# Performance work log

Hardware: AMD Instinct MI355X
Metric: run time of the kernel (lower is better)

The kernel has to match this reference:

```python
import jax, jax.numpy as jnp
import numpy as np
import itertools

BINS_NUM = 35
BINS_SIZE = 9
ORDERS = (2, 3, 4, 5)

def _comb_idx(n, k):
    # combinations with replacement of indices 0..n-1, shape [ncomb, k]
    return np.array(list(itertools.combinations_with_replacement(range(n), k)), dtype=np.int32)

_COMB = {k: _comb_idx(BINS_SIZE, k) for k in ORDERS}


def setup_inputs() -> dict:
    key = jax.random.key(0)
    x = jax.random.normal(key, (1024, BINS_NUM * BINS_SIZE), dtype=jnp.float32)
    return {"x": x}


def reference(x) -> jnp.ndarray:
    B = x.shape[0]
    bins = x.reshape(B, BINS_NUM, BINS_SIZE)          # [B, 35, 9]
    parts = [bins]                                     # 'origin' slice first
    for k in ORDERS:
        idx = jnp.asarray(_COMB[k])                    # [ncomb_k, k]
        gathered = bins[:, :, idx]                     # [B, 35, ncomb_k, k]
        parts.append(jnp.prod(gathered, axis=-1))      # [B, 35, ncomb_k]
    # per-bin concat [origin, de2, de3, de4, de5], then flatten bins -> matches
    # torch's outer concat over bins since bin is the leading concat axis here.
    out = jnp.concatenate(parts, axis=-1)              # [B, 35, 2001]
    return out.reshape(B, -1)                          # [B, 70035]
```

## Files before the change

### kernel.cpp

```cpp
#include <hip/hip_runtime.h>

#define NBIN 35
#define BSZ 9
#define NOUT_PER_BIN 2001

struct PackTab { unsigned pk[NOUT_PER_BIN]; };

constexpr PackTab make_tab() {
    PackTab t{};
    int p = 0;
    constexpr unsigned S = 9;
    for (unsigned a = 0; a < 9; ++a)
        t.pk[p++] = a | (S << 4) | (S << 8) | (S << 12) | (S << 16);
    for (unsigned a = 0; a < 9; ++a)
        for (unsigned b = a; b < 9; ++b)
            t.pk[p++] = a | (b << 4) | (S << 8) | (S << 12) | (S << 16);
    for (unsigned a = 0; a < 9; ++a)
        for (unsigned b = a; b < 9; ++b)
            for (unsigned c = b; c < 9; ++c)
                t.pk[p++] = a | (b << 4) | (c << 8) | (S << 12) | (S << 16);
    for (unsigned a = 0; a < 9; ++a)
        for (unsigned b = a; b < 9; ++b)
            for (unsigned c = b; c < 9; ++c)
                for (unsigned d = c; d < 9; ++d)
                    t.pk[p++] = a | (b << 4) | (c << 8) | (d << 12) | (S << 16);
    for (unsigned a = 0; a < 9; ++a)
        for (unsigned b = a; b < 9; ++b)
            for (unsigned c = b; c < 9; ++c)
                for (unsigned d = c; d < 9; ++d)
                    for (unsigned e = d; e < 9; ++e)
                        t.pk[p++] = a | (b << 4) | (c << 8) | (d << 12) | (e << 16);
    return t;
}

__constant__ PackTab g_tab = make_tab();

__global__ __launch_bounds__(256) void poly_expand_kernel(
        const float* __restrict__ x, float* __restrict__ out, int ntask) {
    __shared__ float vs[4][12];
    const int wave = threadIdx.x >> 6;
    const int lane = threadIdx.x & 63;
    const int task = blockIdx.x * 4 + wave;
    const bool valid = task < ntask;

    if (valid && lane < 10) {
        vs[wave][lane] = (lane < 9) ? x[(size_t)task * BSZ + lane] : 1.0f;
    }
    __syncthreads();
    if (!valid) return;

    const float* v = vs[wave];
    const size_t base = (size_t)task * NOUT_PER_BIN;

    for (int j0 = 0; j0 < NOUT_PER_BIN; j0 += 64) {
        const int j = j0 + lane;
        if (j < NOUT_PER_BIN) {
            const unsigned pk = g_tab.pk[j];
            float p = v[pk & 15u];
            p *= v[(pk >> 4) & 15u];
            p *= v[(pk >> 8) & 15u];
            p *= v[(pk >> 12) & 15u];
            p *= v[(pk >> 16) & 15u];
            out[base + j] = p;
        }
    }
}

extern "C" void kernel_launch(void* const* d_in, const int* in_sizes, int n_in,
                              void* d_out, int out_size, void* d_ws, size_t ws_size,
                              hipStream_t stream) {
    const float* x = (const float*)d_in[0];
    float* out = (float*)d_out;
    const int B = in_sizes[0] / (NBIN * BSZ);
    const int ntask = B * NBIN;
    const int blocks = (ntask + 3) / 4;
    poly_expand_kernel<<<blocks, 256, 0, stream>>>(x, out, ntask);
}
```

Baseline: 60.61 us.

## Compute monomials per-lane with compile-time indices and transpose through LDS

Each lane now owns one bin-task and keeps its 9 values in registers. It evaluates every monomial with indices fixed at compile time, so the constant-table lookups and dynamic LDS indexing go away. Results are staged in a padded LDS tile, transposed, and written out as 16-byte vector stores. The 2001 outputs are split into 9 slices handled by separate waves. This trades heavy code unrolling, instruction-cache pressure and extra LDS traffic for fewer table reads and wider global stores, on a kernel that is write-bandwidth bound.

```diff
diff --git a/kernel.cpp b/kernel.cpp
--- a/kernel.cpp
+++ b/kernel.cpp
@@ -1,78 +1,143 @@
 #include <hip/hip_runtime.h>
+#include <utility>
 
-#define NBIN 35
-#define BSZ 9
-#define NOUT_PER_BIN 2001
+#define NPB  2001
+#define ROWW 65
 
-struct PackTab { unsigned pk[NOUT_PER_BIN]; };
+#define WAVE_SYNC() asm volatile("s_waitcnt lgkmcnt(0)" ::: "memory")
 
-constexpr PackTab make_tab() {
-    PackTab t{};
-    int p = 0;
-    constexpr unsigned S = 9;
-    for (unsigned a = 0; a < 9; ++a)
-        t.pk[p++] = a | (S << 4) | (S << 8) | (S << 12) | (S << 16);
-    for (unsigned a = 0; a < 9; ++a)
-        for (unsigned b = a; b < 9; ++b)
-            t.pk[p++] = a | (b << 4) | (S << 8) | (S << 12) | (S << 16);
-    for (unsigned a = 0; a < 9; ++a)
-        for (unsigned b = a; b < 9; ++b)
-            for (unsigned c = b; c < 9; ++c)
-                t.pk[p++] = a | (b << 4) | (c << 8) | (S << 12) | (S << 16);
-    for (unsigned a = 0; a < 9; ++a)
-        for (unsigned b = a; b < 9; ++b)
-            for (unsigned c = b; c < 9; ++c)
-                for (unsigned d = c; d < 9; ++d)
-                    t.pk[p++] = a | (b << 4) | (c << 8) | (d << 12) | (S << 16);
-    for (unsigned a = 0; a < 9; ++a)
-        for (unsigned b = a; b < 9; ++b)
-            for (unsigned c = b; c < 9; ++c)
-                for (unsigned d = c; d < 9; ++d)
-                    for (unsigned e = d; e < 9; ++e)
-                        t.pk[p++] = a | (b << 4) | (c << 8) | (d << 12) | (e << 16);
-    return t;
+typedef float vfloat4 __attribute__((ext_vector_type(4)));
+
+struct Comp { int o; int ix[5]; };
+
+constexpr long mscount(int n, int k) {
+  if (k <= 0) return 1;
+  long num = 1, den = 1;
+  for (int i = 0; i < k; ++i) { num *= (n + k - 1 - i); den *= (i + 1); }
+  return num / den;
+}
+constexpr Comp comp(int s) {
+  Comp c{1, {0, 0, 0, 0, 0}};
+  int k, r;
+  if (s < 9)        { k = 1; r = s; }
+  else if (s < 54)  { k = 2; r = s - 9; }
+  else if (s < 219) { k = 3; r = s - 54; }
+  else if (s < 714) { k = 4; r = s - 219; }
+  else              { k = 5; r = s - 714; }
+  c.o = k;
+  int cur = 0;
+  for (int pos = 0; pos < k; ++pos) {
+    for (int vv = cur; vv < 9; ++vv) {
+      long cnt = mscount(9 - vv, k - pos - 1);
+      if ((long)r < cnt) { c.ix[pos] = vv; cur = vv; break; }
+      r -= (int)cnt;
+    }
+  }
+  return c;
 }
 
-__constant__ PackTab g_tab = make_tab();
+template<int S0, class F, int... Is>
+__device__ __forceinline__ void unroll_impl(F&& f, std::integer_sequence<int, Is...>) {
+  (f(std::integral_constant<int, S0 + Is>{}), ...);
+}
+template<int S0, int S1, class F>
+__device__ __forceinline__ void unroll_range(F&& f) {
+  unroll_impl<S0>(static_cast<F&&>(f), std::make_integer_sequence<int, S1 - S0>{});
+}
 
-__global__ __launch_bounds__(256) void poly_expand_kernel(
-        const float* __restrict__ x, float* __restrict__ out, int ntask) {
-    __shared__ float vs[4][12];
-    const int wave = threadIdx.x >> 6;
-    const int lane = threadIdx.x & 63;
-    const int task = blockIdx.x * 4 + wave;
-    const bool valid = task < ntask;
+template<int K>
+__device__ __forceinline__ void chunk_write(const float (&v)[9], float* Lb, int lane) {
+  constexpr int S0 = 32 * K;
+  constexpr int NR = (S0 + 32 <= NPB) ? 32 : (NPB - S0);
+  unroll_range<0, NR>([&](auto rc) {
+    constexpr int R = decltype(rc)::value;
+    constexpr Comp C = comp(S0 + R);
+    float p = v[C.ix[0]];
+    if constexpr (C.o >= 2) p *= v[C.ix[1]];
+    if constexpr (C.o >= 3) p *= v[C.ix[2]];
+    if constexpr (C.o >= 4) p *= v[C.ix[3]];
+    if constexpr (C.o >= 5) p *= v[C.ix[4]];
+    Lb[R * ROWW + lane] = p;
+  });
+}
 
-    if (valid && lane < 10) {
-        vs[wave][lane] = (lane < 9) ? x[(size_t)task * BSZ + lane] : 1.0f;
+template<bool LAST>
+__device__ __forceinline__ void readback_store(
+    const float* Lb, float* __restrict__ out, unsigned base,
+    int G, int ntask, int u, int q) {
+  #pragma unroll
+  for (int i = 0; i < 8; ++i) {
+    const int col = 8 * i + u;
+    const int t = G + col;
+    if (t >= ntask) continue;
+    float* const po = out + (unsigned)t * (unsigned)NPB + base;
+    if (!LAST || q < 4) {
+      const float* p = Lb + 4 * q * ROWW + col;
+      vfloat4 w = { p[0], p[ROWW], p[2 * ROWW], p[3 * ROWW] };
+      __builtin_memcpy(po + 4 * q, &w, 16);
+    } else if (q == 4) {
+      po[16] = Lb[16 * ROWW + col];
     }
-    __syncthreads();
-    if (!valid) return;
+  }
+}
 
-    const float* v = vs[wave];
-    const size_t base = (size_t)task * NOUT_PER_BIN;
+template<int SL>
+__device__ __forceinline__ void run_slice(
+    const float (&v)[9], float* Lb, float* __restrict__ out,
+    int G, int ntask, int u, int q, int lane) {
+  unroll_range<SL * 7, SL * 7 + 7>([&](auto kc) {
+    constexpr int K = decltype(kc)::value;
+    chunk_write<K>(v, Lb, lane);
+    WAVE_SYNC();
+    readback_store<(K == 62)>(Lb, out, 32u * (unsigned)K, G, ntask, u, q);
+    WAVE_SYNC();
+  });
+}
 
-    for (int j0 = 0; j0 < NOUT_PER_BIN; j0 += 64) {
-        const int j = j0 + lane;
-        if (j < NOUT_PER_BIN) {
-            const unsigned pk = g_tab.pk[j];
-            float p = v[pk & 15u];
-            p *= v[(pk >> 4) & 15u];
-            p *= v[(pk >> 8) & 15u];
-            p *= v[(pk >> 12) & 15u];
-            p *= v[(pk >> 16) & 15u];
-            out[base + j] = p;
-        }
-    }
+__global__ __launch_bounds__(256) void poly_dfs_kernel(
+    const float* __restrict__ x, float* __restrict__ out,
+    int ntask, int ngroups) {
+  __shared__ float L[4][32 * ROWW];
+  const int wave = threadIdx.x >> 6;
+  const int lane = threadIdx.x & 63;
+  const int wid = blockIdx.x * 4 + wave;
+  const int group = wid / 9;
+  const int slice = wid - group * 9;
+  if (group >= ngroups) return;
+  const int G = group * 64;
+  float* const Lb = L[wave];
+
+  float v[9];
+  {
+    const int t = G + lane;
+    const int tc = (t < ntask) ? t : (ntask - 1);
+    const float* xs = x + (size_t)tc * 9;
+    #pragma unroll
+    for (int i = 0; i < 9; ++i) v[i] = xs[i];
+  }
+  const int u = lane >> 3, q = lane & 7;
+
+  switch (slice) {
+    case 0: run_slice<0>(v, Lb, out, G, ntask, u, q, lane); break;
+    case 1: run_slice<1>(v, Lb, out, G, ntask, u, q, lane); break;
+    case 2: run_slice<2>(v, Lb, out, G, ntask, u, q, lane); break;
+    case 3: run_slice<3>(v, Lb, out, G, ntask, u, q, lane); break;
+    case 4: run_slice<4>(v, Lb, out, G, ntask, u, q, lane); break;
+    case 5: run_slice<5>(v, Lb, out, G, ntask, u, q, lane); break;
+    case 6: run_slice<6>(v, Lb, out, G, ntask, u, q, lane); break;
+    case 7: run_slice<7>(v, Lb, out, G, ntask, u, q, lane); break;
+    default: run_slice<8>(v, Lb, out, G, ntask, u, q, lane); break;
+  }
 }
 
 extern "C" void kernel_launch(void* const* d_in, const int* in_sizes, int n_in,
                               void* d_out, int out_size, void* d_ws, size_t ws_size,
                               hipStream_t stream) {
-    const float* x = (const float*)d_in[0];
-    float* out = (float*)d_out;
-    const int B = in_sizes[0] / (NBIN * BSZ);
-    const int ntask = B * NBIN;
-    const int blocks = (ntask + 3) / 4;
-    poly_expand_kernel<<<blocks, 256, 0, stream>>>(x, out, ntask);
+  const float* x = (const float*)d_in[0];
+  float* out = (float*)d_out;
+  const int ntask = in_sizes[0] / 9;
+  const int ngroups = (ntask + 63) / 64;
+  const int nwaves = ngroups * 9;
+  const int blocks = (nwaves + 3) / 4;
+  poly_dfs_kernel<<<blocks, 256, 0, stream>>>(x, out, ntask, ngroups);
 }
```

Result: slower. 68.73 us (+13.4%).
